# Optimization experiments

Hardware: AMD Instinct MI355X
Metric: run time of the kernel (lower is better)

Reference implementation:

```python
import jax, jax.numpy as jnp
import numpy as np

B, T, E, NH = 32, 512, 128, 16
HD = E // NH


def setup_inputs() -> dict:
    key = jax.random.key(0)
    ks = jax.random.split(key, 20)
    s = 0.05
    inp = {
        'anchor_input': jax.random.normal(ks[0], (B, T, 4), jnp.float32),
        'pos_input': jax.random.normal(ks[1], (B, T, 4), jnp.float32),
        'neg_input': jax.random.normal(ks[2], (B, T, 4), jnp.float32),
        'anchor_len': jax.random.randint(ks[3], (B,), 1, T + 1, jnp.int32),
        'pos_len': jax.random.randint(ks[4], (B,), 1, T + 1, jnp.int32),
        'neg_len': jax.random.randint(ks[5], (B,), 1, T + 1, jnp.int32),
        # GRUCell(input_size=2, hidden=128)
        'gru_w_ih': jax.random.normal(ks[6], (3 * E, 2), jnp.float32) * s,
        'gru_w_hh': jax.random.normal(ks[7], (3 * E, E), jnp.float32) * s,
        'gru_b_ih': jax.random.normal(ks[8], (3 * E,), jnp.float32) * s,
        'gru_b_hh': jax.random.normal(ks[9], (3 * E,), jnp.float32) * s,
        # lookup = Linear(2, 128); position_result = Linear(2, 128)
        'lookup_w': jax.random.normal(ks[10], (E, 2), jnp.float32) * s,
        'lookup_b': jax.random.normal(ks[11], (E,), jnp.float32) * s,
        'posres_w': jax.random.normal(ks[12], (E, 2), jnp.float32) * s,
        'posres_b': jax.random.normal(ks[13], (E,), jnp.float32) * s,
        # MultiheadAttention(128, 16)
        'attn_in_w': jax.random.normal(ks[14], (3 * E, E), jnp.float32) * s,
        'attn_in_b': jax.random.normal(ks[15], (3 * E,), jnp.float32) * s,
        'attn_out_w': jax.random.normal(ks[16], (E, E), jnp.float32) * s,
        'attn_out_b': jax.random.normal(ks[17], (E,), jnp.float32) * s,
        'gamma': jnp.float32(0.5),
    }
    return inp


def _sin_pos_emb(x):
    # FixedAbsolutePositionEmbedding with hidden_size=2, type='fixed':
    # x + [sin(pos), cos(pos)] (inv_freq for dim 2 is just 1.0)
    pos = jnp.arange(x.shape[1], dtype=x.dtype)
    pe = jnp.stack([jnp.sin(pos), jnp.cos(pos)], axis=-1)  # [T, 2]
    return x + pe[None, :, :]


def _gru_last(x, lens, w_ih, w_hh, b_ih, b_hh):
    # x: [B, T, 2] -> last valid hidden per torch GRUCell math
    xg = jnp.einsum('btf,gf->btg', x, w_ih) + b_ih  # [B, T, 3E]

    def step(h, xg_t):
        hg = h @ w_hh.T + b_hh
        xr, xz, xn = jnp.split(xg_t, 3, axis=-1)
        hr, hz, hn = jnp.split(hg, 3, axis=-1)
        r = jax.nn.sigmoid(xr + hr)
        z = jax.nn.sigmoid(xz + hz)
        n = jnp.tanh(xn + r * hn)
        h2 = (1.0 - z) * n + z * h
        return h2, h2

    h0 = jnp.zeros((x.shape[0], w_hh.shape[1]), x.dtype)
    _, outs = jax.lax.scan(step, h0, jnp.swapaxes(xg, 0, 1))  # [T, B, E]
    return outs[lens - 1, jnp.arange(x.shape[0])]  # [B, E]


def _mha(x, in_w, in_b, out_w, out_b):
    qkv = x @ in_w.T + in_b  # [B, T, 3E]
    q, k, v = jnp.split(qkv, 3, axis=-1)
    q = q.reshape(B, T, NH, HD)
    k = k.reshape(B, T, NH, HD)
    v = v.reshape(B, T, NH, HD)
    scores = jnp.einsum('bqhd,bkhd->bhqk', q, k) / np.sqrt(HD).astype(np.float32)
    attn = jax.nn.softmax(scores, axis=-1)
    o = jnp.einsum('bhqk,bkhd->bqhd', attn, v).reshape(B, T, E)
    return o @ out_w.T + out_b


def _embed(inp, lens, p):
    coor, grid = inp[:, :, :2], inp[:, :, 2:]
    coor_embs = _gru_last(coor, lens, p['gru_w_ih'], p['gru_w_hh'], p['gru_b_ih'], p['gru_b_hh'])
    sig = grid @ p['lookup_w'].T + p['lookup_b']
    posg = _sin_pos_emb(grid) @ p['posres_w'].T + p['posres_b']
    m = sig + posg  # [B, T, E]
    attn = _mha(m, p['attn_in_w'], p['attn_in_b'], p['attn_out_w'], p['attn_out_b'])
    grid_embs = jnp.mean(attn, axis=1)
    g = p['gamma']
    return g * coor_embs + (1.0 - g) * grid_embs


def reference(anchor_input, pos_input, neg_input, anchor_len, pos_len, neg_len,
              gru_w_ih, gru_w_hh, gru_b_ih, gru_b_hh, lookup_w, lookup_b,
              posres_w, posres_b, attn_in_w, attn_in_b, attn_out_w, attn_out_b, gamma):
    p = dict(gru_w_ih=gru_w_ih, gru_w_hh=gru_w_hh, gru_b_ih=gru_b_ih, gru_b_hh=gru_b_hh,
             lookup_w=lookup_w, lookup_b=lookup_b, posres_w=posres_w, posres_b=posres_b,
             attn_in_w=attn_in_w, attn_in_b=attn_in_b, attn_out_w=attn_out_w,
             attn_out_b=attn_out_b, gamma=gamma)
    a = _embed(anchor_input, anchor_len, p)
    pe = _embed(pos_input, pos_len, p)
    ne = _embed(neg_input, neg_len, p)
    eps = 1e-6  # matches F.pairwise_distance eps
    pos_d = jnp.exp(-jnp.sqrt(jnp.sum((a - pe + eps) ** 2, axis=-1)))
    neg_d = jnp.exp(-jnp.sqrt(jnp.sum((a - ne + eps) ** 2, axis=-1)))
    return ((a, pe, ne), (pos_d, neg_d))
```

## Files before the change

### kernel.cpp

```cpp
#include <hip/hip_runtime.h>
#include <math.h>

#define BB 32
#define TT 512
#define EE 128
#define NHH 16
#define HDD 8
#define G3 384
#define NGRU 96
#define NATT 192

typedef __attribute__((ext_vector_type(2))) _Float16 half2_t;
typedef __attribute__((ext_vector_type(8))) _Float16 half8_t;

__device__ __forceinline__ float sigmoidf_(float x) {
  return __builtin_amdgcn_rcpf(1.0f + __expf(-x));
}

__device__ __forceinline__ float exp2_(float x) {
#if __has_builtin(__builtin_amdgcn_exp2f)
  return __builtin_amdgcn_exp2f(x);
#else
  return exp2f(x);
#endif
}

__device__ __forceinline__ float fdot2_(half2_t a, half2_t b, float c) {
#if __has_builtin(__builtin_amdgcn_fdot2)
  return __builtin_amdgcn_fdot2(a, b, c, false);
#else
  return fmaf((float)a[0], (float)b[0], fmaf((float)a[1], (float)b[1], c));
#endif
}

__global__ __launch_bounds__(512) void coef_kernel(
    const float* __restrict__ attn_in_w, const float* __restrict__ attn_in_b,
    const float* __restrict__ lookup_w, const float* __restrict__ lookup_b,
    const float* __restrict__ posres_w, const float* __restrict__ posres_b,
    float* __restrict__ coef, float* __restrict__ Mh) {
  int j = threadIdx.x;
  __shared__ float cL[5][G3];
  if (j < G3) {
    float u0 = 0.f, u1 = 0.f, cs = 0.f, cc = 0.f, cb = 0.f;
    const float* wrow = attn_in_w + j * EE;
    for (int e = 0; e < EE; ++e) {
      float w = wrow[e];
      float pw0 = posres_w[e * 2], pw1 = posres_w[e * 2 + 1];
      u0 += w * (lookup_w[e * 2] + pw0);
      u1 += w * (lookup_w[e * 2 + 1] + pw1);
      cs += w * pw0;
      cc += w * pw1;
      cb += w * (lookup_b[e] + posres_b[e]);
    }
    cb += attn_in_b[j];
    coef[0 * G3 + j] = u0;
    coef[1 * G3 + j] = u1;
    coef[2 * G3 + j] = cs;
    coef[3 * G3 + j] = cc;
    coef[4 * G3 + j] = cb;
    cL[0][j] = u0;
    cL[1][j] = u1;
    cL[2][j] = cs;
    cL[3][j] = cc;
    cL[4][j] = cb;
  }
  __syncthreads();
  if (j < NHH * 25) {
    int h = j / 25;
    int ij = j % 25;
    int i = ij / 5, jj = ij % 5;
    const float SCL = 0.35355339059327373f * 1.4426950408889634f;
    float acc = 0.f;
#pragma unroll
    for (int d = 0; d < HDD; ++d)
      acc += cL[i][h * HDD + d] * cL[jj][EE + h * HDD + d];
    Mh[h * 25 + ij] = acc * SCL;
  }
}

__global__ __launch_bounds__(512, 1) void fused_kernel(
    const float* __restrict__ in0, const float* __restrict__ in1,
    const float* __restrict__ in2, const int* __restrict__ len0,
    const int* __restrict__ len1, const int* __restrict__ len2,
    const float* __restrict__ w_ih, const float* __restrict__ w_hh,
    const float* __restrict__ b_ih, const float* __restrict__ b_hh,
    const float* __restrict__ coef, const float* __restrict__ Mh,
    float* __restrict__ coor_embs, float* __restrict__ ohat) {
  int tid = threadIdx.x;
  if (blockIdx.x < NGRU) {
    if (tid >= 256) return;
    int blk = blockIdx.x;
    int s = blk >> 5;
    int b = blk & 31;
    const float* inp = (s == 0) ? in0 : (s == 1) ? in1 : in2;
    const int* lenp = (s == 0) ? len0 : (s == 1) ? len1 : len2;
    int len = lenp[b];
    int e = tid >> 1;
    int kp = tid & 1;

    __shared__ __align__(16) _Float16 hbh[2][EE];
    __shared__ __align__(16) float xst[TT * 2];

    for (int t = tid; t < TT; t += 256) {
      float4 v = *(const float4*)(inp + ((size_t)b * TT + t) * 4);
      xst[t * 2] = v.x;
      xst[t * 2 + 1] = v.y;
    }
    if (tid < EE) hbh[0][tid] = (_Float16)0.0f;

    int rr = e, rz = e + 128, rn = e + 256;
    half2_t wr[32], wz[32], wn[32];
    {
      const float4* pr = (const float4*)(w_hh + (size_t)rr * EE + 64 * kp);
      const float4* pz = (const float4*)(w_hh + (size_t)rz * EE + 64 * kp);
      const float4* pn = (const float4*)(w_hh + (size_t)rn * EE + 64 * kp);
#pragma unroll
      for (int i = 0; i < 16; ++i) {
        float4 a = pr[i];
        wr[2 * i][0] = (_Float16)a.x; wr[2 * i][1] = (_Float16)a.y;
        wr[2 * i + 1][0] = (_Float16)a.z; wr[2 * i + 1][1] = (_Float16)a.w;
        float4 c = pz[i];
        wz[2 * i][0] = (_Float16)c.x; wz[2 * i][1] = (_Float16)c.y;
        wz[2 * i + 1][0] = (_Float16)c.z; wz[2 * i + 1][1] = (_Float16)c.w;
        float4 d = pn[i];
        wn[2 * i][0] = (_Float16)d.x; wn[2 * i][1] = (_Float16)d.y;
        wn[2 * i + 1][0] = (_Float16)d.z; wn[2 * i + 1][1] = (_Float16)d.w;
      }
    }
    float br = b_ih[rr] + b_hh[rr];
    float bz = b_ih[rz] + b_hh[rz];
    float bn = b_ih[rn];
    float bhn = b_hh[rn];
    float wir0 = w_ih[rr * 2], wir1 = w_ih[rr * 2 + 1];
    float wiz0 = w_ih[rz * 2], wiz1 = w_ih[rz * 2 + 1];
    float win0 = w_ih[rn * 2], win1 = w_ih[rn * 2 + 1];

    float hold = 0.0f;
    __syncthreads();

#pragma unroll 1
    for (int t = 0; t < len; ++t) {
      const half8_t* hp = (const half8_t*)(hbh[t & 1] + 64 * kp);
      half2_t h2[32];
#pragma unroll
      for (int m = 0; m < 8; ++m) {
        half8_t H = hp[m];
        h2[4 * m][0] = H[0]; h2[4 * m][1] = H[1];
        h2[4 * m + 1][0] = H[2]; h2[4 * m + 1][1] = H[3];
        h2[4 * m + 2][0] = H[4]; h2[4 * m + 2][1] = H[5];
        h2[4 * m + 3][0] = H[6]; h2[4 * m + 3][1] = H[7];
      }
      float x0 = xst[t * 2], x1 = xst[t * 2 + 1];

      float ar0 = 0.f, ar1 = 0.f, az0 = 0.f, az1 = 0.f, an0 = 0.f, an1 = 0.f;
#pragma unroll
      for (int jj = 0; jj < 32; jj += 2) {
        ar0 = fdot2_(wr[jj], h2[jj], ar0);
        ar1 = fdot2_(wr[jj + 1], h2[jj + 1], ar1);
        az0 = fdot2_(wz[jj], h2[jj], az0);
        az1 = fdot2_(wz[jj + 1], h2[jj + 1], az1);
        an0 = fdot2_(wn[jj], h2[jj], an0);
        an1 = fdot2_(wn[jj + 1], h2[jj + 1], an1);
      }
      float hr = ar0 + ar1, hz = az0 + az1, hn = an0 + an1;

      hr += __shfl_xor(hr, 1);
      hz += __shfl_xor(hz, 1);
      hn += __shfl_xor(hn, 1);

      float r = sigmoidf_(br + wir0 * x0 + wir1 * x1 + hr);
      float z = sigmoidf_(bz + wiz0 * x0 + wiz1 * x1 + hz);
      float targ = bn + win0 * x0 + win1 * x1 + r * (bhn + hn);
      float ex = __expf(2.0f * targ);
      float n = 1.0f - 2.0f * __builtin_amdgcn_rcpf(ex + 1.0f);
      hold = n + z * (hold - n);
      if (kp == 0) hbh[(t & 1) ^ 1][e] = (_Float16)hold;
      __syncthreads();
    }
    if (kp == 0) coor_embs[(size_t)blk * EE + e] = hold;
  } else {
    int a = blockIdx.x - NGRU;
    int s = a / 64;
    int rem = a - s * 64;
    int b = rem >> 1;
    int hg = rem & 1;
    const float* inp = (s == 0) ? in0 : (s == 1) ? in1 : in2;
    int wave = tid >> 6;
    int lane = tid & 63;
    int h = hg * 8 + wave;

    __shared__ __align__(16) float4 phiL[TT];

    {
      int t = tid;
      float ft = (float)t;
      float st = sinf(ft);
      float ct = cosf(ft);
      float4 g = *(const float4*)(inp + ((size_t)b * TT + t) * 4);
      phiL[t] = make_float4(g.z, g.w, st, ct);
    }

    float M[25];
#pragma unroll
    for (int i = 0; i < 25; ++i) M[i] = Mh[h * 25 + i];
    __syncthreads();

    float4 p[8];
#pragma unroll
    for (int j = 0; j < 8; ++j) p[j] = phiL[lane + 64 * j];

    float Z[8];
    float N0[8], N1[8], N2[8], N3[8];
#pragma unroll
    for (int j = 0; j < 8; ++j) {
      Z[j] = 0.f; N0[j] = 0.f; N1[j] = 0.f; N2[j] = 0.f; N3[j] = 0.f;
    }

#pragma unroll 1
    for (int k = 0; k < TT; ++k) {
      float4 f = phiL[k];
      float m0 = fmaf(M[0], f.x, fmaf(M[1], f.y, fmaf(M[2], f.z, fmaf(M[3], f.w, M[4]))));
      float m1 = fmaf(M[5], f.x, fmaf(M[6], f.y, fmaf(M[7], f.z, fmaf(M[8], f.w, M[9]))));
      float m2 = fmaf(M[10], f.x, fmaf(M[11], f.y, fmaf(M[12], f.z, fmaf(M[13], f.w, M[14]))));
      float m3 = fmaf(M[15], f.x, fmaf(M[16], f.y, fmaf(M[17], f.z, fmaf(M[18], f.w, M[19]))));
      float m4 = fmaf(M[20], f.x, fmaf(M[21], f.y, fmaf(M[22], f.z, fmaf(M[23], f.w, M[24]))));
#pragma unroll
      for (int j = 0; j < 8; ++j) {
        float e0 = exp2_(fmaf(p[j].x, m0, fmaf(p[j].y, m1, fmaf(p[j].z, m2, fmaf(p[j].w, m3, m4)))));
        Z[j] += e0;
        N0[j] = fmaf(e0, f.x, N0[j]);
        N1[j] = fmaf(e0, f.y, N1[j]);
        N2[j] = fmaf(e0, f.z, N2[j]);
        N3[j] = fmaf(e0, f.w, N3[j]);
      }
    }

    float od0 = 0.f, od1 = 0.f, od2 = 0.f, od3 = 0.f;
#pragma unroll
    for (int j = 0; j < 8; ++j) {
      float rz = __builtin_amdgcn_rcpf(Z[j] * (float)TT);
      od0 = fmaf(N0[j], rz, od0);
      od1 = fmaf(N1[j], rz, od1);
      od2 = fmaf(N2[j], rz, od2);
      od3 = fmaf(N3[j], rz, od3);
    }
#pragma unroll
    for (int off = 32; off >= 1; off >>= 1) {
      od0 += __shfl_xor(od0, off, 64);
      od1 += __shfl_xor(od1, off, 64);
      od2 += __shfl_xor(od2, off, 64);
      od3 += __shfl_xor(od3, off, 64);
    }
    if (lane < HDD) {
      int jv = 2 * EE + h * HDD + lane;
      float o = coef[jv] * od0 + coef[G3 + jv] * od1 + coef[2 * G3 + jv] * od2 +
                coef[3 * G3 + jv] * od3 + coef[4 * G3 + jv];
      int abk = s * 512 + b * 16 + h;
      ohat[(size_t)abk * HDD + lane] = o;
    }
  }
}

__global__ __launch_bounds__(128) void finalize_kernel(
    const float* __restrict__ attn_out_w, const float* __restrict__ attn_out_b,
    const float* __restrict__ ohat, const float* __restrict__ coor_embs,
    const float* __restrict__ gamma_p, float* __restrict__ out) {
  int blk = blockIdx.x;
  int e = threadIdx.x;
  __shared__ float ov[EE];
  ov[e] = ohat[(size_t)blk * EE + e];
  __syncthreads();
  float acc = attn_out_b[e];
  const float* wrow = attn_out_w + (size_t)e * EE;
#pragma unroll 8
  for (int f = 0; f < EE; ++f) acc += wrow[f] * ov[f];
  float g = gamma_p[0];
  out[(size_t)blk * EE + e] = g * coor_embs[(size_t)blk * EE + e] + (1.0f - g) * acc;
}

__global__ void dist_kernel(float* __restrict__ out) {
  int i = threadIdx.x;
  int b = i & 31;
  int neg = i >> 5;
  const float* a = out + (size_t)b * EE;
  const float* x = out + (size_t)(1 + neg) * BB * EE + (size_t)b * EE;
  float sum = 0.f;
  for (int e = 0; e < EE; ++e) {
    float d = a[e] - x[e] + 1e-6f;
    sum += d * d;
  }
  out[3 * BB * EE + neg * BB + b] = expf(-sqrtf(sum));
}

extern "C" void kernel_launch(void* const* d_in, const int* in_sizes, int n_in,
                              void* d_out, int out_size, void* d_ws, size_t ws_size,
                              hipStream_t stream) {
  const float* a_in = (const float*)d_in[0];
  const float* p_in = (const float*)d_in[1];
  const float* ng_in = (const float*)d_in[2];
  const int* a_len = (const int*)d_in[3];
  const int* p_len = (const int*)d_in[4];
  const int* ng_len = (const int*)d_in[5];
  const float* w_ih = (const float*)d_in[6];
  const float* w_hh = (const float*)d_in[7];
  const float* b_ih = (const float*)d_in[8];
  const float* b_hh = (const float*)d_in[9];
  const float* lookup_w = (const float*)d_in[10];
  const float* lookup_b = (const float*)d_in[11];
  const float* posres_w = (const float*)d_in[12];
  const float* posres_b = (const float*)d_in[13];
  const float* attn_in_w = (const float*)d_in[14];
  const float* attn_in_b = (const float*)d_in[15];
  const float* attn_out_w = (const float*)d_in[16];
  const float* attn_out_b = (const float*)d_in[17];
  const float* gamma_p = (const float*)d_in[18];
  float* out = (float*)d_out;

  float* coef = (float*)d_ws;
  float* Mh = coef + 2048;
  float* ohat = Mh + 512;
  float* cemb = ohat + 12288;

  hipLaunchKernelGGL(coef_kernel, dim3(1), dim3(512), 0, stream, attn_in_w,
                     attn_in_b, lookup_w, lookup_b, posres_w, posres_b, coef, Mh);
  hipLaunchKernelGGL(fused_kernel, dim3(NGRU + NATT), dim3(512), 0, stream, a_in,
                     p_in, ng_in, a_len, p_len, ng_len, w_ih, w_hh, b_ih, b_hh,
                     coef, Mh, cemb, ohat);
  hipLaunchKernelGGL(finalize_kernel, dim3(96), dim3(128), 0, stream, attn_out_w,
                     attn_out_b, ohat, cemb, gamma_p, out);
  hipLaunchKernelGGL(dist_kernel, dim3(1), dim3(64), 0, stream, out);
}
```

Before: 327.1 us.

## Batch GRU recurrence across 16 sequences per block using MFMA matmuls

The GRU recurrence used to run as one block per sequence, with each thread doing packed fp16 dot products. It now runs one block per 16 batch sequences, 6 GRU blocks in total, and computes the hidden-to-hidden matvec as a 16x16x32 MFMA GEMM with weights held in registers as A fragments. Each block loops to the maximum length in its group and captures each sequence's final state at its own length. This removes the per-step scalar dot-product cost and frees CUs for the attention blocks. In exchange, every block runs up to the longest sequence in its 16, inputs are stored in fp16, and fewer blocks carry the serial critical path. Shared memory is unified into one buffer and the launch-bound occupancy hint of 1 is dropped.

```diff
diff --git a/kernel.cpp b/kernel.cpp
--- a/kernel.cpp
+++ b/kernel.cpp
@@ -7,11 +7,13 @@
 #define NHH 16
 #define HDD 8
 #define G3 384
-#define NGRU 96
+#define NGRU 6
 #define NATT 192
 
 typedef __attribute__((ext_vector_type(2))) _Float16 half2_t;
+typedef __attribute__((ext_vector_type(4))) _Float16 half4_t;
 typedef __attribute__((ext_vector_type(8))) _Float16 half8_t;
+typedef __attribute__((ext_vector_type(4))) float f32x4;
 
 __device__ __forceinline__ float sigmoidf_(float x) {
   return __builtin_amdgcn_rcpf(1.0f + __expf(-x));
@@ -25,12 +27,15 @@
 #endif
 }
 
-__device__ __forceinline__ float fdot2_(half2_t a, half2_t b, float c) {
-#if __has_builtin(__builtin_amdgcn_fdot2)
-  return __builtin_amdgcn_fdot2(a, b, c, false);
-#else
-  return fmaf((float)a[0], (float)b[0], fmaf((float)a[1], (float)b[1], c));
-#endif
+__device__ __forceinline__ half8_t ldfrag(const float* p) {
+  float4 f0 = *(const float4*)p;
+  float4 f1 = *(const float4*)(p + 4);
+  half8_t r;
+  r[0] = (_Float16)f0.x; r[1] = (_Float16)f0.y;
+  r[2] = (_Float16)f0.z; r[3] = (_Float16)f0.w;
+  r[4] = (_Float16)f1.x; r[5] = (_Float16)f1.y;
+  r[6] = (_Float16)f1.z; r[7] = (_Float16)f1.w;
+  return r;
 }
 
 __global__ __launch_bounds__(512) void coef_kernel(
@@ -78,7 +83,7 @@
   }
 }
 
-__global__ __launch_bounds__(512, 1) void fused_kernel(
+__global__ __launch_bounds__(512) void fused_kernel(
     const float* __restrict__ in0, const float* __restrict__ in1,
     const float* __restrict__ in2, const int* __restrict__ len0,
     const int* __restrict__ len1, const int* __restrict__ len2,
@@ -86,98 +91,136 @@
     const float* __restrict__ b_ih, const float* __restrict__ b_hh,
     const float* __restrict__ coef, const float* __restrict__ Mh,
     float* __restrict__ coor_embs, float* __restrict__ ohat) {
+  __shared__ __align__(16) unsigned char smem[41472];
   int tid = threadIdx.x;
   if (blockIdx.x < NGRU) {
-    if (tid >= 256) return;
     int blk = blockIdx.x;
-    int s = blk >> 5;
-    int b = blk & 31;
+    int s = blk >> 1;
+    int hb = blk & 1;
     const float* inp = (s == 0) ? in0 : (s == 1) ? in1 : in2;
     const int* lenp = (s == 0) ? len0 : (s == 1) ? len1 : len2;
-    int len = lenp[b];
-    int e = tid >> 1;
-    int kp = tid & 1;
-
-    __shared__ __align__(16) _Float16 hbh[2][EE];
-    __shared__ __align__(16) float xst[TT * 2];
-
-    for (int t = tid; t < TT; t += 256) {
-      float4 v = *(const float4*)(inp + ((size_t)b * TT + t) * 4);
-      xst[t * 2] = v.x;
-      xst[t * 2 + 1] = v.y;
-    }
-    if (tid < EE) hbh[0][tid] = (_Float16)0.0f;
-
-    int rr = e, rz = e + 128, rn = e + 256;
-    half2_t wr[32], wz[32], wn[32];
-    {
-      const float4* pr = (const float4*)(w_hh + (size_t)rr * EE + 64 * kp);
-      const float4* pz = (const float4*)(w_hh + (size_t)rz * EE + 64 * kp);
-      const float4* pn = (const float4*)(w_hh + (size_t)rn * EE + 64 * kp);
-#pragma unroll
-      for (int i = 0; i < 16; ++i) {
-        float4 a = pr[i];
-        wr[2 * i][0] = (_Float16)a.x; wr[2 * i][1] = (_Float16)a.y;
-        wr[2 * i + 1][0] = (_Float16)a.z; wr[2 * i + 1][1] = (_Float16)a.w;
-        float4 c = pz[i];
-        wz[2 * i][0] = (_Float16)c.x; wz[2 * i][1] = (_Float16)c.y;
-        wz[2 * i + 1][0] = (_Float16)c.z; wz[2 * i + 1][1] = (_Float16)c.w;
-        float4 d = pn[i];
-        wn[2 * i][0] = (_Float16)d.x; wn[2 * i][1] = (_Float16)d.y;
-        wn[2 * i + 1][0] = (_Float16)d.z; wn[2 * i + 1][1] = (_Float16)d.w;
-      }
-    }
-    float br = b_ih[rr] + b_hh[rr];
-    float bz = b_ih[rz] + b_hh[rz];
-    float bn = b_ih[rn];
-    float bhn = b_hh[rn];
-    float wir0 = w_ih[rr * 2], wir1 = w_ih[rr * 2 + 1];
-    float wiz0 = w_ih[rz * 2], wiz1 = w_ih[rz * 2 + 1];
-    float win0 = w_ih[rn * 2], win1 = w_ih[rn * 2 + 1];
-
-    float hold = 0.0f;
+    int w = tid >> 6;
+    int l = tid & 63;
+    int c = l & 15;
+    int q = l >> 4;
+
+    _Float16* Ht = (_Float16*)smem;
+    half2_t* xst = (half2_t*)(smem + 8704);
+
+    for (int idx = tid; idx < 16 * TT; idx += 512) {
+      int t = idx & 511;
+      int bl = idx >> 9;
+      float4 v = *(const float4*)(inp + ((size_t)(hb * 16 + bl) * TT + t) * 4);
+      half2_t xv;
+      xv[0] = (_Float16)v.x;
+      xv[1] = (_Float16)v.y;
+      xst[t * 16 + bl] = xv;
+    }
+    for (int idx = tid; idx < 16 * 136; idx += 512) Ht[idx] = (_Float16)0.0f;
+
+    int lenc = lenp[hb * 16 + c];
+    int maxlen = lenc;
+#pragma unroll
+    for (int off = 1; off < 16; off <<= 1) {
+      int o = __shfl_xor(maxlen, off, 64);
+      maxlen = maxlen > o ? maxlen : o;
+    }
+
+    const float* pR = w_hh + ((size_t)(0 + 16 * w + c)) * EE + 8 * q;
+    const float* pZ = w_hh + ((size_t)(128 + 16 * w + c)) * EE + 8 * q;
+    const float* pN = w_hh + ((size_t)(256 + 16 * w + c)) * EE + 8 * q;
+    half8_t aR0 = ldfrag(pR), aR1 = ldfrag(pR + 32), aR2 = ldfrag(pR + 64), aR3 = ldfrag(pR + 96);
+    half8_t aZ0 = ldfrag(pZ), aZ1 = ldfrag(pZ + 32), aZ2 = ldfrag(pZ + 64), aZ3 = ldfrag(pZ + 96);
+    half8_t aN0 = ldfrag(pN), aN1 = ldfrag(pN + 32), aN2 = ldfrag(pN + 64), aN3 = ldfrag(pN + 96);
+
+    int e0 = 16 * w + 4 * q;
+    float br_[4], bz_[4], bn_[4], bhn_[4];
+    float wir0_[4], wir1_[4], wiz0_[4], wiz1_[4], win0_[4], win1_[4];
+#pragma unroll
+    for (int rr = 0; rr < 4; ++rr) {
+      int er = e0 + rr;
+      br_[rr] = b_ih[er] + b_hh[er];
+      bz_[rr] = b_ih[128 + er] + b_hh[128 + er];
+      bn_[rr] = b_ih[256 + er];
+      bhn_[rr] = b_hh[256 + er];
+      wir0_[rr] = w_ih[er * 2];
+      wir1_[rr] = w_ih[er * 2 + 1];
+      wiz0_[rr] = w_ih[(128 + er) * 2];
+      wiz1_[rr] = w_ih[(128 + er) * 2 + 1];
+      win0_[rr] = w_ih[(256 + er) * 2];
+      win1_[rr] = w_ih[(256 + er) * 2 + 1];
+    }
+
+    float hold0 = 0.f, hold1 = 0.f, hold2 = 0.f, hold3 = 0.f;
+    float hs0 = 0.f, hs1 = 0.f, hs2 = 0.f, hs3 = 0.f;
     __syncthreads();
 
+    int cur = 0;
 #pragma unroll 1
-    for (int t = 0; t < len; ++t) {
-      const half8_t* hp = (const half8_t*)(hbh[t & 1] + 64 * kp);
-      half2_t h2[32];
-#pragma unroll
-      for (int m = 0; m < 8; ++m) {
-        half8_t H = hp[m];
-        h2[4 * m][0] = H[0]; h2[4 * m][1] = H[1];
-        h2[4 * m + 1][0] = H[2]; h2[4 * m + 1][1] = H[3];
-        h2[4 * m + 2][0] = H[4]; h2[4 * m + 2][1] = H[5];
-        h2[4 * m + 3][0] = H[6]; h2[4 * m + 3][1] = H[7];
-      }
-      float x0 = xst[t * 2], x1 = xst[t * 2 + 1];
-
-      float ar0 = 0.f, ar1 = 0.f, az0 = 0.f, az1 = 0.f, an0 = 0.f, an1 = 0.f;
-#pragma unroll
-      for (int jj = 0; jj < 32; jj += 2) {
-        ar0 = fdot2_(wr[jj], h2[jj], ar0);
-        ar1 = fdot2_(wr[jj + 1], h2[jj + 1], ar1);
-        az0 = fdot2_(wz[jj], h2[jj], az0);
-        az1 = fdot2_(wz[jj + 1], h2[jj + 1], az1);
-        an0 = fdot2_(wn[jj], h2[jj], an0);
-        an1 = fdot2_(wn[jj + 1], h2[jj + 1], an1);
-      }
-      float hr = ar0 + ar1, hz = az0 + az1, hn = an0 + an1;
-
-      hr += __shfl_xor(hr, 1);
-      hz += __shfl_xor(hz, 1);
-      hn += __shfl_xor(hn, 1);
-
-      float r = sigmoidf_(br + wir0 * x0 + wir1 * x1 + hr);
-      float z = sigmoidf_(bz + wiz0 * x0 + wiz1 * x1 + hz);
-      float targ = bn + win0 * x0 + win1 * x1 + r * (bhn + hn);
-      float ex = __expf(2.0f * targ);
-      float n = 1.0f - 2.0f * __builtin_amdgcn_rcpf(ex + 1.0f);
-      hold = n + z * (hold - n);
-      if (kp == 0) hbh[(t & 1) ^ 1][e] = (_Float16)hold;
+    for (int t = 0; t < maxlen; ++t) {
+      const _Float16* hrow = Ht + cur * 2176 + c * 136 + 8 * q;
+      half8_t b0 = *(const half8_t*)(hrow);
+      half8_t b1 = *(const half8_t*)(hrow + 32);
+      half8_t b2 = *(const half8_t*)(hrow + 64);
+      half8_t b3 = *(const half8_t*)(hrow + 96);
+
+      f32x4 aR = {0.f, 0.f, 0.f, 0.f};
+      f32x4 aZ = {0.f, 0.f, 0.f, 0.f};
+      f32x4 aN = {0.f, 0.f, 0.f, 0.f};
+      aR = __builtin_amdgcn_mfma_f32_16x16x32_f16(aR0, b0, aR, 0, 0, 0);
+      aZ = __builtin_amdgcn_mfma_f32_16x16x32_f16(aZ0, b0, aZ, 0, 0, 0);
+      aN = __builtin_amdgcn_mfma_f32_16x16x32_f16(aN0, b0, aN, 0, 0, 0);
+      aR = __builtin_amdgcn_mfma_f32_16x16x32_f16(aR1, b1, aR, 0, 0, 0);
+      aZ = __builtin_amdgcn_mfma_f32_16x16x32_f16(aZ1, b1, aZ, 0, 0, 0);
+      aN = __builtin_amdgcn_mfma_f32_16x16x32_f16(aN1, b1, aN, 0, 0, 0);
+      aR = __builtin_amdgcn_mfma_f32_16x16x32_f16(aR2, b2, aR, 0, 0, 0);
+      aZ = __builtin_amdgcn_mfma_f32_16x16x32_f16(aZ2, b2, aZ, 0, 0, 0);
+      aN = __builtin_amdgcn_mfma_f32_16x16x32_f16(aN2, b2, aN, 0, 0, 0);
+      aR = __builtin_amdgcn_mfma_f32_16x16x32_f16(aR3, b3, aR, 0, 0, 0);
+      aZ = __builtin_amdgcn_mfma_f32_16x16x32_f16(aZ3, b3, aZ, 0, 0, 0);
+      aN = __builtin_amdgcn_mfma_f32_16x16x32_f16(aN3, b3, aN, 0, 0, 0);
+
+      half2_t xv = xst[t * 16 + c];
+      float x0 = (float)xv[0], x1 = (float)xv[1];
+
+      float rg0 = sigmoidf_(br_[0] + wir0_[0] * x0 + wir1_[0] * x1 + aR[0]);
+      float zg0 = sigmoidf_(bz_[0] + wiz0_[0] * x0 + wiz1_[0] * x1 + aZ[0]);
+      float tg0 = bn_[0] + win0_[0] * x0 + win1_[0] * x1 + rg0 * (bhn_[0] + aN[0]);
+      float ng0 = 1.0f - 2.0f * __builtin_amdgcn_rcpf(__expf(2.0f * tg0) + 1.0f);
+      hold0 = ng0 + zg0 * (hold0 - ng0);
+
+      float rg1 = sigmoidf_(br_[1] + wir0_[1] * x0 + wir1_[1] * x1 + aR[1]);
+      float zg1 = sigmoidf_(bz_[1] + wiz0_[1] * x0 + wiz1_[1] * x1 + aZ[1]);
+      float tg1 = bn_[1] + win0_[1] * x0 + win1_[1] * x1 + rg1 * (bhn_[1] + aN[1]);
+      float ng1 = 1.0f - 2.0f * __builtin_amdgcn_rcpf(__expf(2.0f * tg1) + 1.0f);
+      hold1 = ng1 + zg1 * (hold1 - ng1);
+
+      float rg2 = sigmoidf_(br_[2] + wir0_[2] * x0 + wir1_[2] * x1 + aR[2]);
+      float zg2 = sigmoidf_(bz_[2] + wiz0_[2] * x0 + wiz1_[2] * x1 + aZ[2]);
+      float tg2 = bn_[2] + win0_[2] * x0 + win1_[2] * x1 + rg2 * (bhn_[2] + aN[2]);
+      float ng2 = 1.0f - 2.0f * __builtin_amdgcn_rcpf(__expf(2.0f * tg2) + 1.0f);
+      hold2 = ng2 + zg2 * (hold2 - ng2);
+
+      float rg3 = sigmoidf_(br_[3] + wir0_[3] * x0 + wir1_[3] * x1 + aR[3]);
+      float zg3 = sigmoidf_(bz_[3] + wiz0_[3] * x0 + wiz1_[3] * x1 + aZ[3]);
+      float tg3 = bn_[3] + win0_[3] * x0 + win1_[3] * x1 + rg3 * (bhn_[3] + aN[3]);
+      float ng3 = 1.0f - 2.0f * __builtin_amdgcn_rcpf(__expf(2.0f * tg3) + 1.0f);
+      hold3 = ng3 + zg3 * (hold3 - ng3);
+
+      if (t == lenc - 1) { hs0 = hold0; hs1 = hold1; hs2 = hold2; hs3 = hold3; }
+
+      half4_t hp;
+      hp[0] = (_Float16)hold0;
+      hp[1] = (_Float16)hold1;
+      hp[2] = (_Float16)hold2;
+      hp[3] = (_Float16)hold3;
+      *(half4_t*)(Ht + (cur ^ 1) * 2176 + c * 136 + e0) = hp;
       __syncthreads();
-    }
-    if (kp == 0) coor_embs[(size_t)blk * EE + e] = hold;
+      cur ^= 1;
+    }
+    float4 o;
+    o.x = hs0; o.y = hs1; o.z = hs2; o.w = hs3;
+    *(float4*)(coor_embs + ((size_t)(s * 32 + hb * 16 + c)) * EE + e0) = o;
   } else {
     int a = blockIdx.x - NGRU;
     int s = a / 64;
@@ -189,7 +232,7 @@
     int lane = tid & 63;
     int h = hg * 8 + wave;
 
-    __shared__ __align__(16) float4 phiL[TT];
+    float4* phiL = (float4*)smem;
 
     {
       int t = tid;
```

Result: slower. 404.9 us (+23.8%).
